# Kernel optimization log

Measured on AMD Instinct MI355X. Metric: run time of the kernel, lower is better.

## Reference

```python
import jax, jax.numpy as jnp
import numpy as np

MAX_DEGREE = 5
NUM_LAYERS = 2


def setup_inputs() -> dict:
    key = jax.random.key(0)
    ks = jax.random.split(key, 10)
    N, F, H, C, E = 200000, 128, 64, 40, 3200000
    x = jax.random.normal(ks[0], (N, F), dtype=jnp.float32)
    edge_index = jax.random.randint(ks[1], (2, E), 0, N, dtype=jnp.int32)
    # torch Linear init ~ U(-1/sqrt(fan_in), 1/sqrt(fan_in)); scaled normals are fine for a baseline
    W1 = jax.random.normal(ks[2], (F, H), dtype=jnp.float32) / np.sqrt(F)
    b1 = jax.random.normal(ks[3], (H,), dtype=jnp.float32) * 0.01
    relW = jax.random.normal(ks[4], (NUM_LAYERS, MAX_DEGREE + 1, H, H), dtype=jnp.float32) / np.sqrt(H)
    relb = jax.random.normal(ks[5], (NUM_LAYERS, MAX_DEGREE + 1, H), dtype=jnp.float32) * 0.01
    Wout = jax.random.normal(ks[6], (H, C), dtype=jnp.float32) / np.sqrt(H)
    bout = jax.random.normal(ks[7], (C,), dtype=jnp.float32) * 0.01
    fuse = jnp.full((NUM_LAYERS,), 1.0 / (NUM_LAYERS + 1), dtype=jnp.float32)
    return {"x": x, "edge_index": edge_index, "W1": W1, "b1": b1,
            "relW": relW, "relb": relb, "Wout": Wout, "bout": bout, "fuse": fuse}


def reference(x, edge_index, W1, b1, relW, relb, Wout, bout, fuse):
    N = x.shape[0]
    src, dst = edge_index[0], edge_index[1]
    loop_mask = (src != dst)  # remove_self_loops
    # degree on target nodes (flow='source_to_target'), clamped to max_degree
    deg = jax.ops.segment_sum(loop_mask.astype(jnp.int32), dst, num_segments=N)
    deg = jnp.clip(deg, 0, MAX_DEGREE)
    node_idx = jnp.arange(N)

    h = jax.nn.relu(x @ W1 + b1)  # dropout is identity in eval mode
    x_first = h
    for i in range(NUM_LAYERS):
        # scatter-add aggregation; self loops added back (root_weight=False)
        msg = jnp.where(loop_mask[:, None], h[src], 0.0)  # [E, H]
        agg = jax.ops.segment_sum(msg, dst, num_segments=N) + h  # [N, H]
        # degree-bucketed linear: compute all 6 buckets, select per node
        all_out = jnp.einsum('nd,kdo->kno', agg, relW[i]) + relb[i][:, None, :]  # [6, N, H]
        conv = all_out[deg, node_idx]  # [N, H]
        h = conv + fuse[i] * x_first
    logits = h @ Wout + bout
    return jax.nn.log_softmax(logits, axis=-1)
```

## Files before the change

kernel.cpp:

```cpp
#include <hip/hip_runtime.h>
#include <cmath>
#include <cstddef>

#define F_IN 128
#define H_DIM 64
#define C_OUT 40
#define MAXDEG 5
#define EPB 16

typedef __attribute__((ext_vector_type(8))) _Float16 half8;
typedef __attribute__((ext_vector_type(4))) _Float16 half4;
typedef __attribute__((ext_vector_type(4))) float fv4;

__device__ __forceinline__ half4 u2h(uint2 u) { return __builtin_bit_cast(half4, u); }
__device__ __forceinline__ uint2 h2u(half4 v) { return __builtin_bit_cast(uint2, v); }


__global__ __launch_bounds__(256) void k_scatter(const int* __restrict__ src,
                                                 const int* __restrict__ dst,
                                                 int E, int NB, int stride,
                                                 int* __restrict__ gcnt,
                                                 unsigned int* __restrict__ ebuf) {
    __shared__ int hist[256];
    __shared__ int base[256];
    int tid = threadIdx.x;
    if (tid < NB) hist[tid] = 0;
    __syncthreads();
    int e0 = blockIdx.x * (256 * EPB);
    int es[EPB], ed[EPB];
#pragma unroll
    for (int i = 0; i < EPB; ++i) {
        int e = e0 + i * 256 + tid;
        int s = -1, d = -1;
        if (e < E) { s = src[e]; d = dst[e]; }
        es[i] = s; ed[i] = d;
        if (d >= 0 && s != d) atomicAdd(&hist[d >> 10], 1);
    }
    __syncthreads();
    if (tid < NB) {
        int c = hist[tid];
        base[tid] = c ? atomicAdd(&gcnt[tid], c) : 0;
        hist[tid] = 0;
    }
    __syncthreads();
#pragma unroll
    for (int i = 0; i < EPB; ++i) {
        int s = es[i], d = ed[i];
        if (d >= 0 && s != d) {
            int b = d >> 10;
            int p = base[b] + atomicAdd(&hist[b], 1);
            if (p < stride)
                ebuf[(size_t)b * stride + p] = ((unsigned)(d & 1023) << 20) | (unsigned)s;
        }
    }
}

__global__ __launch_bounds__(1024) void k_build(const unsigned int* __restrict__ ebuf,
                                                const int* __restrict__ gcnt, int stride, int N,
                                                int* __restrict__ row, int* __restrict__ cnt,
                                                int* __restrict__ col, int* __restrict__ list,
                                                int* __restrict__ listctr) {
    __shared__ int lcnt[1024];
    __shared__ int lcur[1024];
    int bk = blockIdx.x;
    int n0 = bk << 10;
    int tid = threadIdx.x;
    int ebase = bk * stride;
    int ec = min(gcnt[bk], stride);
    int eend = ebase + ec;
    lcnt[tid] = 0;
    __syncthreads();
    for (int e = ebase + tid; e < eend; e += 1024)
        atomicAdd(&lcnt[ebuf[e] >> 20], 1);
    __syncthreads();
    int v = lcnt[tid];
    lcur[tid] = v;
    __syncthreads();
    for (int off = 1; off < 1024; off <<= 1) {
        int t = (tid >= off) ? lcur[tid - off] : 0;
        __syncthreads();
        lcur[tid] += t;
        __syncthreads();
    }
    int ex = lcur[tid] - v;
    __syncthreads();
    lcur[tid] = ebase + ex;
    int n = n0 + tid;
    if (n < N) {
        row[n] = ebase + ex;
        cnt[n] = v;
        if (v < MAXDEG) {
            int p = atomicAdd(listctr, 1);
            list[p] = n;
        }
    }
    __syncthreads();
    for (int e = ebase + tid; e < eend; e += 1024) {
        unsigned edv = ebuf[e];
        int dl = edv >> 20;
        int p = atomicAdd(&lcur[dl], 1);
        col[p] = (int)(edv & 0xFFFFF);
    }
}

__global__ __launch_bounds__(256) void k_lin1(const float* __restrict__ x,
                                              const float* __restrict__ W1,
                                              const float* __restrict__ b1,
                                              _Float16* __restrict__ h, int N) {
    __shared__ _Float16 Wl[4 * 4 * 64 * 8];
    int tid = threadIdx.x;
    for (int idx = tid; idx < 4 * 4 * 64 * 8; idx += 256) {
        int j = idx & 7, ln = (idx >> 3) & 63, ks = (idx >> 9) & 3, t = idx >> 11;
        int k = ks * 32 + (ln >> 4) * 8 + j;
        int n = t * 16 + (ln & 15);
        Wl[idx] = (_Float16)W1[k * H_DIM + n];
    }
    __syncthreads();

    int wave = tid >> 6, lane = tid & 63;
    int tile = blockIdx.x * 4 + wave;
    int row0 = tile * 16;
    if (row0 >= N) return;
    int m = lane & 15, quad = lane >> 4;
    int row = row0 + m;
    if (row >= N) row = N - 1;

    half8 a[4];
    const float* xr = x + (size_t)row * F_IN + quad * 8;
#pragma unroll
    for (int ks = 0; ks < 4; ++ks) {
        fv4 lo = *(const fv4*)(xr + ks * 32);
        fv4 hi = *(const fv4*)(xr + ks * 32 + 4);
        half8 av;
#pragma unroll
        for (int j = 0; j < 4; ++j) av[j] = (_Float16)lo[j];
#pragma unroll
        for (int j = 0; j < 4; ++j) av[4 + j] = (_Float16)hi[j];
        a[ks] = av;
    }

    fv4 acc[4];
#pragma unroll
    for (int t = 0; t < 4; ++t) acc[t] = (fv4){0.f, 0.f, 0.f, 0.f};
#pragma unroll
    for (int ks = 0; ks < 4; ++ks) {
#pragma unroll
        for (int t = 0; t < 4; ++t) {
            half8 b = *(const half8*)&Wl[(((t * 4 + ks) * 64) + lane) * 8];
            acc[t] = __builtin_amdgcn_mfma_f32_16x16x32_f16(a[ks], b, acc[t], 0, 0, 0);
        }
    }
#pragma unroll
    for (int t = 0; t < 4; ++t) {
        int n = t * 16 + m;
        float bias = b1[n];
#pragma unroll
        for (int reg = 0; reg < 4; ++reg) {
            int r = row0 + quad * 4 + reg;
            if (r < N) {
                float v = acc[t][reg] + bias;
                h[(size_t)r * H_DIM + n] = (_Float16)fmaxf(v, 0.f);
            }
        }
    }
}

__global__ void k_agg(const _Float16* __restrict__ hin, const int* __restrict__ row,
                      const int* __restrict__ cnt, const int* __restrict__ col,
                      _Float16* __restrict__ agg, int N) {
    int gid = blockIdx.x * blockDim.x + threadIdx.x;
    int n = gid >> 6, lane = gid & 63;
    if (n >= N) return;
    int g = lane >> 4;
    int f = lane & 15;
    int base = row[n];
    int c = cnt[n];
    const uint2* hv = (const uint2*)hin;
    half4 acc = u2h((uint2){0u, 0u});
    for (int j0 = 0; j0 < c; j0 += 64) {
        int idx = j0 + lane;
        int myc = (idx < c) ? col[base + idx] : 0;
        int mm = min(64, c - j0);
        int t = 0;
        for (; t + 8 <= mm; t += 8) {
            int s0 = __shfl(myc, t + g);
            int s1 = __shfl(myc, t + 4 + g);
            uint2 u0 = hv[(size_t)s0 * 16 + f];
            uint2 u1 = hv[(size_t)s1 * 16 + f];
            acc += u2h(u0);
            acc += u2h(u1);
        }
        for (; t < mm; t += 4) {
            int e = t + g;
            bool val = (e < mm);
            int s = __shfl(myc, val ? e : 0);
            uint2 u = hv[(size_t)(val ? s : n) * 16 + f];
            if (!val) u = (uint2){0u, 0u};
            acc += u2h(u);
        }
    }
    {
        uint2 t1 = h2u(acc);
        t1.x = __shfl_xor(t1.x, 16); t1.y = __shfl_xor(t1.y, 16);
        acc += u2h(t1);
        uint2 t2 = h2u(acc);
        t2.x = __shfl_xor(t2.x, 32); t2.y = __shfl_xor(t2.y, 32);
        acc += u2h(t2);
    }
    acc += u2h(hv[(size_t)n * 16 + f]);
    if (g == 0)
        ((uint2*)agg)[(size_t)n * 16 + f] = h2u(acc);
}

__global__ __launch_bounds__(256) void k_bucket(const _Float16* __restrict__ agg,
                                                const float* __restrict__ relW,
                                                const float* __restrict__ relb,
                                                const float* __restrict__ fuse, int layer,
                                                const _Float16* __restrict__ xfirst,
                                                _Float16* __restrict__ h, int N) {
    __shared__ _Float16 Wl[4 * 2 * 64 * 8];
    const float* W = relW + (size_t)(layer * 6 + MAXDEG) * (H_DIM * H_DIM);
    int tid = threadIdx.x;
    for (int idx = tid; idx < 4 * 2 * 64 * 8; idx += 256) {
        int j = idx & 7, ln = (idx >> 3) & 63, ks = (idx >> 9) & 1, t = idx >> 10;
        int k = ks * 32 + (ln >> 4) * 8 + j;
        int n = t * 16 + (ln & 15);
        Wl[idx] = (_Float16)W[k * H_DIM + n];
    }
    __syncthreads();

    int wave = tid >> 6, lane = tid & 63;
    int tile = blockIdx.x * 4 + wave;
    int row0 = tile * 16;
    if (row0 >= N) return;
    int m = lane & 15, quad = lane >> 4;
    int row = row0 + m;
    if (row >= N) row = N - 1;

    half8 a[2];
#pragma unroll
    for (int ks = 0; ks < 2; ++ks)
        a[ks] = *(const half8*)(agg + (size_t)row * H_DIM + ks * 32 + quad * 8);

    fv4 acc[4];
#pragma unroll
    for (int t = 0; t < 4; ++t) acc[t] = (fv4){0.f, 0.f, 0.f, 0.f};
#pragma unroll
    for (int ks = 0; ks < 2; ++ks) {
#pragma unroll
        for (int t = 0; t < 4; ++t) {
            half8 b = *(const half8*)&Wl[(((t * 2 + ks) * 64) + lane) * 8];
            acc[t] = __builtin_amdgcn_mfma_f32_16x16x32_f16(a[ks], b, acc[t], 0, 0, 0);
        }
    }
    float fu = fuse[layer];
    const float* bias = relb + (layer * 6 + MAXDEG) * H_DIM;
#pragma unroll
    for (int t = 0; t < 4; ++t) {
        int n = t * 16 + m;
        float bv = bias[n];
#pragma unroll
        for (int reg = 0; reg < 4; ++reg) {
            int r = row0 + quad * 4 + reg;
            if (r < N) {
                float v = acc[t][reg] + bv + fu * (float)xfirst[(size_t)r * H_DIM + n];
                h[(size_t)r * H_DIM + n] = (_Float16)v;
            }
        }
    }
}

__global__ void k_fixup(const _Float16* __restrict__ agg, const int* __restrict__ list,
                        const int* __restrict__ listctr, const int* __restrict__ cnt,
                        const float* __restrict__ relW, const float* __restrict__ relb,
                        const float* __restrict__ fuse, int layer,
                        const _Float16* __restrict__ xfirst,
                        _Float16* __restrict__ h) {
    int gid = blockIdx.x * blockDim.x + threadIdx.x;
    int wave = gid >> 6, lane = gid & 63;
    int nwaves = (gridDim.x * blockDim.x) >> 6;
    int M = *listctr;
    float fu = fuse[layer];
    for (int i = wave; i < M; i += nwaves) {
        int n = list[i];
        int d = cnt[n];
        const float* W = relW + (size_t)(layer * 6 + d) * (H_DIM * H_DIM);
        float a = (float)agg[(size_t)n * H_DIM + lane];
        float acc = relb[(layer * 6 + d) * H_DIM + lane];
#pragma unroll 16
        for (int k = 0; k < 64; ++k)
            acc = fmaf(__shfl(a, k), W[k * H_DIM + lane], acc);
        acc += fu * (float)xfirst[(size_t)n * H_DIM + lane];
        h[(size_t)n * H_DIM + lane] = (_Float16)acc;
    }
}

__global__ __launch_bounds__(256) void k_out(const _Float16* __restrict__ h,
                                             const float* __restrict__ Wout,
                                             const float* __restrict__ bout,
                                             float* __restrict__ out, int N) {
    __shared__ _Float16 Wl[3 * 2 * 64 * 8];
    int tid = threadIdx.x;
    for (int idx = tid; idx < 3 * 2 * 64 * 8; idx += 256) {
        int j = idx & 7, ln = (idx >> 3) & 63, ks = (idx >> 9) & 1, t = idx >> 10;
        int k = ks * 32 + (ln >> 4) * 8 + j;
        int n = t * 16 + (ln & 15);
        Wl[idx] = (n < C_OUT) ? (_Float16)Wout[k * C_OUT + n] : (_Float16)0.f;
    }
    __syncthreads();

    int wave = tid >> 6, lane = tid & 63;
    int tile = blockIdx.x * 4 + wave;
    int row0 = tile * 16;
    if (row0 >= N) return;
    int m = lane & 15, quad = lane >> 4;
    int row = row0 + m;
    if (row >= N) row = N - 1;

    half8 a[2];
#pragma unroll
    for (int ks = 0; ks < 2; ++ks)
        a[ks] = *(const half8*)(h + (size_t)row * H_DIM + ks * 32 + quad * 8);

    fv4 acc[3];
#pragma unroll
    for (int t = 0; t < 3; ++t) acc[t] = (fv4){0.f, 0.f, 0.f, 0.f};
#pragma unroll
    for (int ks = 0; ks < 2; ++ks) {
#pragma unroll
        for (int t = 0; t < 3; ++t) {
            half8 b = *(const half8*)&Wl[(((t * 2 + ks) * 64) + lane) * 8];
            acc[t] = __builtin_amdgcn_mfma_f32_16x16x32_f16(a[ks], b, acc[t], 0, 0, 0);
        }
    }
    bool v2 = (m < 8);
    float b0 = bout[m], b1v = bout[16 + m], b2v = v2 ? bout[32 + m] : 0.f;
#pragma unroll
    for (int reg = 0; reg < 4; ++reg) {
        int r = row0 + quad * 4 + reg;
        float l0 = acc[0][reg] + b0;
        float l1 = acc[1][reg] + b1v;
        float l2 = v2 ? (acc[2][reg] + b2v) : -INFINITY;
        float mx = fmaxf(fmaxf(l0, l1), l2);
#pragma unroll
        for (int off = 1; off < 16; off <<= 1) mx = fmaxf(mx, __shfl_xor(mx, off));
        float s = expf(l0 - mx) + expf(l1 - mx) + (v2 ? expf(l2 - mx) : 0.f);
#pragma unroll
        for (int off = 1; off < 16; off <<= 1) s += __shfl_xor(s, off);
        float ls = logf(s);
        if (r < N) {
            out[(size_t)r * C_OUT + m] = l0 - mx - ls;
            out[(size_t)r * C_OUT + 16 + m] = l1 - mx - ls;
            if (v2) out[(size_t)r * C_OUT + 32 + m] = l2 - mx - ls;
        }
    }
}

extern "C" void kernel_launch(void* const* d_in, const int* in_sizes, int n_in,
                              void* d_out, int out_size, void* d_ws, size_t ws_size,
                              hipStream_t stream) {
    const float* x    = (const float*)d_in[0];
    const int*   ei   = (const int*)d_in[1];
    const float* W1   = (const float*)d_in[2];
    const float* b1   = (const float*)d_in[3];
    const float* relW = (const float*)d_in[4];
    const float* relb = (const float*)d_in[5];
    const float* Wout = (const float*)d_in[6];
    const float* bout = (const float*)d_in[7];
    const float* fuse = (const float*)d_in[8];
    float* out = (float*)d_out;

    int N = in_sizes[0] / F_IN;
    int E = in_sizes[1] / 2;
    const int* src = ei;
    const int* dst = ei + E;
    int NB = (N + 1023) >> 10;
    int mean = (E + NB - 1) / NB;
    int stride = mean + mean / 8 + 512;

    char* w = (char*)d_ws;
    auto alloc = [&](size_t bytes) {
        char* p = w;
        w += (bytes + 255) & ~(size_t)255;
        return p;
    };
    int* cnt     = (int*)alloc((size_t)N * 4);
    int* row     = (int*)alloc((size_t)N * 4);
    int* list    = (int*)alloc((size_t)N * 4);
    int* listctr = (int*)alloc(256);
    int* gcnt    = (int*)alloc(1024 * 4);
    int* col     = (int*)alloc((size_t)NB * stride * 4);
    _Float16* h0   = (_Float16*)alloc((size_t)N * H_DIM * 2);
    _Float16* h1   = (_Float16*)alloc((size_t)N * H_DIM * 2);
    _Float16* aggb = (_Float16*)alloc((size_t)N * H_DIM * 2);
    unsigned int* ebuf = (unsigned int*)h0;

    hipMemsetAsync(gcnt, 0, 1024 * 4, stream);
    hipMemsetAsync(listctr, 0, 4, stream);

    k_scatter<<<(E + 256 * EPB - 1) / (256 * EPB), 256, 0, stream>>>(src, dst, E, NB, stride, gcnt, ebuf);
    k_build<<<NB, 1024, 0, stream>>>(ebuf, gcnt, stride, N, row, cnt, col, list, listctr);

    int tiles = (N + 15) / 16;
    int gblk = (tiles + 3) / 4;
    int ablk = ((size_t)N * 64 + 255) / 256;

    k_lin1<<<gblk, 256, 0, stream>>>(x, W1, b1, h0, N);

    k_agg<<<ablk, 256, 0, stream>>>(h0, row, cnt, col, aggb, N);
    k_bucket<<<gblk, 256, 0, stream>>>(aggb, relW, relb, fuse, 0, h0, h1, N);
    k_fixup<<<16, 256, 0, stream>>>(aggb, list, listctr, cnt, relW, relb, fuse, 0, h0, h1);

    k_agg<<<ablk, 256, 0, stream>>>(h1, row, cnt, col, aggb, N);
    k_bucket<<<gblk, 256, 0, stream>>>(aggb, relW, relb, fuse, 1, h0, h1, N);
    k_fixup<<<16, 256, 0, stream>>>(aggb, list, listctr, cnt, relW, relb, fuse, 1, h0, h1);

    k_out<<<gblk, 256, 0, stream>>>(h1, Wout, bout, out, N);
}
```

Measured before the change: 532.4 us.

## Fuse low-degree fixup into bucket GEMM, fuse output head, and repack aggregation

The separate fixup kernels are removed. Each bucket block now patches its own low-degree rows using a shared-memory list, so the global list and its atomics are gone. The final layer's bucket transform is fused with the output projection and log-softmax through a shared-memory staging tile, which drops the h1 round trip and one launch. Aggregation now gives each wave four nodes (16 lanes each) and pads with a zero sentinel row to avoid shuffle reductions. CSR bins shrink to 512 nodes. The cost is per-block serial fixup work and lane divergence when nodes in a wave have uneven degrees.

```diff
diff --git a/kernel.cpp b/kernel.cpp
--- a/kernel.cpp
+++ b/kernel.cpp
@@ -21,10 +21,10 @@
                                                  int E, int NB, int stride,
                                                  int* __restrict__ gcnt,
                                                  unsigned int* __restrict__ ebuf) {
-    __shared__ int hist[256];
-    __shared__ int base[256];
+    __shared__ int hist[512];
+    __shared__ int base[512];
     int tid = threadIdx.x;
-    if (tid < NB) hist[tid] = 0;
+    for (int i = tid; i < NB; i += 256) hist[i] = 0;
     __syncthreads();
     int e0 = blockIdx.x * (256 * EPB);
     int es[EPB], ed[EPB];
@@ -34,49 +34,48 @@
         int s = -1, d = -1;
         if (e < E) { s = src[e]; d = dst[e]; }
         es[i] = s; ed[i] = d;
-        if (d >= 0 && s != d) atomicAdd(&hist[d >> 10], 1);
-    }
-    __syncthreads();
-    if (tid < NB) {
-        int c = hist[tid];
-        base[tid] = c ? atomicAdd(&gcnt[tid], c) : 0;
-        hist[tid] = 0;
+        if (d >= 0 && s != d) atomicAdd(&hist[d >> 9], 1);
+    }
+    __syncthreads();
+    for (int i = tid; i < NB; i += 256) {
+        int c = hist[i];
+        base[i] = c ? atomicAdd(&gcnt[i], c) : 0;
+        hist[i] = 0;
     }
     __syncthreads();
 #pragma unroll
     for (int i = 0; i < EPB; ++i) {
         int s = es[i], d = ed[i];
         if (d >= 0 && s != d) {
-            int b = d >> 10;
+            int b = d >> 9;
             int p = base[b] + atomicAdd(&hist[b], 1);
             if (p < stride)
-                ebuf[(size_t)b * stride + p] = ((unsigned)(d & 1023) << 20) | (unsigned)s;
-        }
-    }
-}
-
-__global__ __launch_bounds__(1024) void k_build(const unsigned int* __restrict__ ebuf,
-                                                const int* __restrict__ gcnt, int stride, int N,
-                                                int* __restrict__ row, int* __restrict__ cnt,
-                                                int* __restrict__ col, int* __restrict__ list,
-                                                int* __restrict__ listctr) {
-    __shared__ int lcnt[1024];
-    __shared__ int lcur[1024];
+                ebuf[(size_t)b * stride + p] = ((unsigned)(d & 511) << 20) | (unsigned)s;
+        }
+    }
+}
+
+__global__ __launch_bounds__(512) void k_build(const unsigned int* __restrict__ ebuf,
+                                               const int* __restrict__ gcnt, int stride, int N,
+                                               int* __restrict__ row, int* __restrict__ cnt,
+                                               int* __restrict__ col) {
+    __shared__ int lcnt[512];
+    __shared__ int lcur[512];
     int bk = blockIdx.x;
-    int n0 = bk << 10;
+    int n0 = bk << 9;
     int tid = threadIdx.x;
     int ebase = bk * stride;
     int ec = min(gcnt[bk], stride);
     int eend = ebase + ec;
     lcnt[tid] = 0;
     __syncthreads();
-    for (int e = ebase + tid; e < eend; e += 1024)
+    for (int e = ebase + tid; e < eend; e += 512)
         atomicAdd(&lcnt[ebuf[e] >> 20], 1);
     __syncthreads();
     int v = lcnt[tid];
     lcur[tid] = v;
     __syncthreads();
-    for (int off = 1; off < 1024; off <<= 1) {
+    for (int off = 1; off < 512; off <<= 1) {
         int t = (tid >= off) ? lcur[tid - off] : 0;
         __syncthreads();
         lcur[tid] += t;
@@ -89,13 +88,9 @@
     if (n < N) {
         row[n] = ebase + ex;
         cnt[n] = v;
-        if (v < MAXDEG) {
-            int p = atomicAdd(listctr, 1);
-            list[p] = n;
-        }
-    }
-    __syncthreads();
-    for (int e = ebase + tid; e < eend; e += 1024) {
+    }
+    __syncthreads();
+    for (int e = ebase + tid; e < eend; e += 512) {
         unsigned edv = ebuf[e];
         int dl = edv >> 20;
         int p = atomicAdd(&lcur[dl], 1);
@@ -106,9 +101,14 @@
 __global__ __launch_bounds__(256) void k_lin1(const float* __restrict__ x,
                                               const float* __restrict__ W1,
                                               const float* __restrict__ b1,
-                                              _Float16* __restrict__ h, int N) {
+                                              _Float16* __restrict__ h,
+                                              _Float16* __restrict__ hz2, int N) {
     __shared__ _Float16 Wl[4 * 4 * 64 * 8];
     int tid = threadIdx.x;
+    if (blockIdx.x == 0 && tid < 64) {
+        h[(size_t)N * H_DIM + tid] = (_Float16)0.f;
+        hz2[(size_t)N * H_DIM + tid] = (_Float16)0.f;
+    }
     for (int idx = tid; idx < 4 * 4 * 64 * 8; idx += 256) {
         int j = idx & 7, ln = (idx >> 3) & 63, ks = (idx >> 9) & 3, t = idx >> 11;
         int k = ks * 32 + (ln >> 4) * 8 + j;
@@ -168,59 +168,60 @@
 __global__ void k_agg(const _Float16* __restrict__ hin, const int* __restrict__ row,
                       const int* __restrict__ cnt, const int* __restrict__ col,
                       _Float16* __restrict__ agg, int N) {
-    int gid = blockIdx.x * blockDim.x + threadIdx.x;
-    int n = gid >> 6, lane = gid & 63;
-    if (n >= N) return;
-    int g = lane >> 4;
-    int f = lane & 15;
-    int base = row[n];
-    int c = cnt[n];
+    int wid = (blockIdx.x * blockDim.x + threadIdx.x) >> 6;
+    int lane = threadIdx.x & 63;
+    int g = lane >> 4, fl = lane & 15, gl = g << 4;
+    int n = wid * 4 + g;
+    bool nv = (n < N);
+    int nn = nv ? n : (N - 1);
+    int base = row[nn];
+    int c = nv ? cnt[nn] : 0;
     const uint2* hv = (const uint2*)hin;
+    int cmax = c;
+    cmax = max(cmax, __shfl_xor(cmax, 16));
+    cmax = max(cmax, __shfl_xor(cmax, 32));
     half4 acc = u2h((uint2){0u, 0u});
-    for (int j0 = 0; j0 < c; j0 += 64) {
-        int idx = j0 + lane;
-        int myc = (idx < c) ? col[base + idx] : 0;
-        int mm = min(64, c - j0);
+    for (int j0 = 0; j0 < cmax; j0 += 16) {
+        int idx = j0 + fl;
+        int myc = (idx < c) ? col[base + idx] : N;
+        int tmax = min(16, cmax - j0);
         int t = 0;
-        for (; t + 8 <= mm; t += 8) {
-            int s0 = __shfl(myc, t + g);
-            int s1 = __shfl(myc, t + 4 + g);
-            uint2 u0 = hv[(size_t)s0 * 16 + f];
-            uint2 u1 = hv[(size_t)s1 * 16 + f];
-            acc += u2h(u0);
-            acc += u2h(u1);
-        }
-        for (; t < mm; t += 4) {
-            int e = t + g;
-            bool val = (e < mm);
-            int s = __shfl(myc, val ? e : 0);
-            uint2 u = hv[(size_t)(val ? s : n) * 16 + f];
-            if (!val) u = (uint2){0u, 0u};
-            acc += u2h(u);
-        }
-    }
-    {
-        uint2 t1 = h2u(acc);
-        t1.x = __shfl_xor(t1.x, 16); t1.y = __shfl_xor(t1.y, 16);
-        acc += u2h(t1);
-        uint2 t2 = h2u(acc);
-        t2.x = __shfl_xor(t2.x, 32); t2.y = __shfl_xor(t2.y, 32);
-        acc += u2h(t2);
-    }
-    acc += u2h(hv[(size_t)n * 16 + f]);
-    if (g == 0)
-        ((uint2*)agg)[(size_t)n * 16 + f] = h2u(acc);
+        for (; t + 4 <= tmax; t += 4) {
+            int s0 = __shfl(myc, gl + t);
+            int s1 = __shfl(myc, gl + t + 1);
+            int s2 = __shfl(myc, gl + t + 2);
+            int s3 = __shfl(myc, gl + t + 3);
+            uint2 u0 = hv[(size_t)s0 * 16 + fl];
+            uint2 u1 = hv[(size_t)s1 * 16 + fl];
+            uint2 u2 = hv[(size_t)s2 * 16 + fl];
+            uint2 u3 = hv[(size_t)s3 * 16 + fl];
+            half4 p01 = u2h(u0) + u2h(u1);
+            half4 p23 = u2h(u2) + u2h(u3);
+            acc += (p01 + p23);
+        }
+        for (; t < tmax; ++t) {
+            int s = __shfl(myc, gl + t);
+            acc += u2h(hv[(size_t)s * 16 + fl]);
+        }
+    }
+    acc += u2h(hv[(size_t)nn * 16 + fl]);
+    if (nv)
+        ((uint2*)agg)[(size_t)nn * 16 + fl] = h2u(acc);
 }
 
 __global__ __launch_bounds__(256) void k_bucket(const _Float16* __restrict__ agg,
+                                                const int* __restrict__ cnt,
                                                 const float* __restrict__ relW,
                                                 const float* __restrict__ relb,
                                                 const float* __restrict__ fuse, int layer,
                                                 const _Float16* __restrict__ xfirst,
                                                 _Float16* __restrict__ h, int N) {
     __shared__ _Float16 Wl[4 * 2 * 64 * 8];
+    __shared__ int flist[64];
+    __shared__ int fn;
     const float* W = relW + (size_t)(layer * 6 + MAXDEG) * (H_DIM * H_DIM);
     int tid = threadIdx.x;
+    if (tid == 0) fn = 0;
     for (int idx = tid; idx < 4 * 2 * 64 * 8; idx += 256) {
         int j = idx & 7, ln = (idx >> 3) & 63, ks = (idx >> 9) & 1, t = idx >> 10;
         int k = ks * 32 + (ln >> 4) * 8 + j;
@@ -230,12 +231,12 @@
     __syncthreads();
 
     int wave = tid >> 6, lane = tid & 63;
-    int tile = blockIdx.x * 4 + wave;
-    int row0 = tile * 16;
-    if (row0 >= N) return;
+    int row0 = blockIdx.x * 64 + wave * 16;
     int m = lane & 15, quad = lane >> 4;
     int row = row0 + m;
     if (row >= N) row = N - 1;
+    float fu = fuse[layer];
+    const float* bias = relb + (layer * 6 + MAXDEG) * H_DIM;
 
     half8 a[2];
 #pragma unroll
@@ -246,15 +247,29 @@
 #pragma unroll
     for (int t = 0; t < 4; ++t) acc[t] = (fv4){0.f, 0.f, 0.f, 0.f};
 #pragma unroll
-    for (int ks = 0; ks < 2; ++ks) {
+    for (int ks = 0; ks < 2; ++ks)
 #pragma unroll
         for (int t = 0; t < 4; ++t) {
             half8 b = *(const half8*)&Wl[(((t * 2 + ks) * 64) + lane) * 8];
             acc[t] = __builtin_amdgcn_mfma_f32_16x16x32_f16(a[ks], b, acc[t], 0, 0, 0);
         }
-    }
-    float fu = fuse[layer];
-    const float* bias = relb + (layer * 6 + MAXDEG) * H_DIM;
+
+    int cr[4];
+#pragma unroll
+    for (int reg = 0; reg < 4; ++reg) {
+        int r = row0 + quad * 4 + reg;
+        cr[reg] = (r < N) ? cnt[r] : MAXDEG;
+    }
+    if (m == 0) {
+#pragma unroll
+        for (int reg = 0; reg < 4; ++reg) {
+            int r = row0 + quad * 4 + reg;
+            if (r < N && cr[reg] < MAXDEG) {
+                int p = atomicAdd(&fn, 1);
+                if (p < 64) flist[p] = wave * 16 + quad * 4 + reg;
+            }
+        }
+    }
 #pragma unroll
     for (int t = 0; t < 4; ++t) {
         int n = t * 16 + m;
@@ -262,85 +277,153 @@
 #pragma unroll
         for (int reg = 0; reg < 4; ++reg) {
             int r = row0 + quad * 4 + reg;
-            if (r < N) {
+            if (r < N && cr[reg] >= MAXDEG) {
                 float v = acc[t][reg] + bv + fu * (float)xfirst[(size_t)r * H_DIM + n];
                 h[(size_t)r * H_DIM + n] = (_Float16)v;
             }
         }
     }
-}
-
-__global__ void k_fixup(const _Float16* __restrict__ agg, const int* __restrict__ list,
-                        const int* __restrict__ listctr, const int* __restrict__ cnt,
-                        const float* __restrict__ relW, const float* __restrict__ relb,
-                        const float* __restrict__ fuse, int layer,
-                        const _Float16* __restrict__ xfirst,
-                        _Float16* __restrict__ h) {
-    int gid = blockIdx.x * blockDim.x + threadIdx.x;
-    int wave = gid >> 6, lane = gid & 63;
-    int nwaves = (gridDim.x * blockDim.x) >> 6;
-    int M = *listctr;
-    float fu = fuse[layer];
-    for (int i = wave; i < M; i += nwaves) {
-        int n = list[i];
-        int d = cnt[n];
-        const float* W = relW + (size_t)(layer * 6 + d) * (H_DIM * H_DIM);
-        float a = (float)agg[(size_t)n * H_DIM + lane];
-        float acc = relb[(layer * 6 + d) * H_DIM + lane];
-#pragma unroll 16
+    __syncthreads();
+    int M = min(fn, 64);
+    for (int i = wave; i < M; i += 4) {
+        int rl = flist[i];
+        int r = blockIdx.x * 64 + rl;
+        int d = cnt[r];
+        const float* Wd = relW + (size_t)(layer * 6 + d) * (H_DIM * H_DIM);
+        float av = (float)agg[(size_t)r * H_DIM + lane];
+        float accf = relb[(layer * 6 + d) * H_DIM + lane];
         for (int k = 0; k < 64; ++k)
-            acc = fmaf(__shfl(a, k), W[k * H_DIM + lane], acc);
-        acc += fu * (float)xfirst[(size_t)n * H_DIM + lane];
-        h[(size_t)n * H_DIM + lane] = (_Float16)acc;
-    }
-}
-
-__global__ __launch_bounds__(256) void k_out(const _Float16* __restrict__ h,
-                                             const float* __restrict__ Wout,
-                                             const float* __restrict__ bout,
-                                             float* __restrict__ out, int N) {
-    __shared__ _Float16 Wl[3 * 2 * 64 * 8];
+            accf = fmaf(__shfl(av, k), Wd[k * H_DIM + lane], accf);
+        accf += fu * (float)xfirst[(size_t)r * H_DIM + lane];
+        h[(size_t)r * H_DIM + lane] = (_Float16)accf;
+    }
+}
+
+#define HB 80
+__global__ __launch_bounds__(256) void k_bucket_out(const _Float16* __restrict__ agg,
+                                                    const int* __restrict__ cnt,
+                                                    const float* __restrict__ relW,
+                                                    const float* __restrict__ relb,
+                                                    const float* __restrict__ fuse,
+                                                    const _Float16* __restrict__ xfirst,
+                                                    const float* __restrict__ Wout,
+                                                    const float* __restrict__ bout,
+                                                    float* __restrict__ out, int N) {
+    __shared__ _Float16 Wl[4 * 2 * 64 * 8];
+    __shared__ _Float16 Wo[3 * 2 * 64 * 8];
+    __shared__ _Float16 hbuf[64 * HB];
+    __shared__ int flist[64];
+    __shared__ int fn;
+    const int layer = 1;
+    const float* W = relW + (size_t)(layer * 6 + MAXDEG) * (H_DIM * H_DIM);
     int tid = threadIdx.x;
+    if (tid == 0) fn = 0;
+    for (int idx = tid; idx < 4 * 2 * 64 * 8; idx += 256) {
+        int j = idx & 7, ln = (idx >> 3) & 63, ks = (idx >> 9) & 1, t = idx >> 10;
+        int k = ks * 32 + (ln >> 4) * 8 + j;
+        int n = t * 16 + (ln & 15);
+        Wl[idx] = (_Float16)W[k * H_DIM + n];
+    }
     for (int idx = tid; idx < 3 * 2 * 64 * 8; idx += 256) {
         int j = idx & 7, ln = (idx >> 3) & 63, ks = (idx >> 9) & 1, t = idx >> 10;
         int k = ks * 32 + (ln >> 4) * 8 + j;
         int n = t * 16 + (ln & 15);
-        Wl[idx] = (n < C_OUT) ? (_Float16)Wout[k * C_OUT + n] : (_Float16)0.f;
+        Wo[idx] = (n < C_OUT) ? (_Float16)Wout[k * C_OUT + n] : (_Float16)0.f;
     }
     __syncthreads();
 
     int wave = tid >> 6, lane = tid & 63;
-    int tile = blockIdx.x * 4 + wave;
-    int row0 = tile * 16;
-    if (row0 >= N) return;
+    int row0 = blockIdx.x * 64 + wave * 16;
     int m = lane & 15, quad = lane >> 4;
     int row = row0 + m;
     if (row >= N) row = N - 1;
+    float fu = fuse[layer];
+    const float* bias = relb + (layer * 6 + MAXDEG) * H_DIM;
 
     half8 a[2];
 #pragma unroll
     for (int ks = 0; ks < 2; ++ks)
-        a[ks] = *(const half8*)(h + (size_t)row * H_DIM + ks * 32 + quad * 8);
-
-    fv4 acc[3];
-#pragma unroll
-    for (int t = 0; t < 3; ++t) acc[t] = (fv4){0.f, 0.f, 0.f, 0.f};
-#pragma unroll
-    for (int ks = 0; ks < 2; ++ks) {
-#pragma unroll
-        for (int t = 0; t < 3; ++t) {
+        a[ks] = *(const half8*)(agg + (size_t)row * H_DIM + ks * 32 + quad * 8);
+
+    fv4 acc[4];
+#pragma unroll
+    for (int t = 0; t < 4; ++t) acc[t] = (fv4){0.f, 0.f, 0.f, 0.f};
+#pragma unroll
+    for (int ks = 0; ks < 2; ++ks)
+#pragma unroll
+        for (int t = 0; t < 4; ++t) {
             half8 b = *(const half8*)&Wl[(((t * 2 + ks) * 64) + lane) * 8];
             acc[t] = __builtin_amdgcn_mfma_f32_16x16x32_f16(a[ks], b, acc[t], 0, 0, 0);
         }
-    }
+
+    int cr[4];
+#pragma unroll
+    for (int reg = 0; reg < 4; ++reg) {
+        int r = row0 + quad * 4 + reg;
+        cr[reg] = (r < N) ? cnt[r] : MAXDEG;
+    }
+    if (m == 0) {
+#pragma unroll
+        for (int reg = 0; reg < 4; ++reg) {
+            int r = row0 + quad * 4 + reg;
+            if (r < N && cr[reg] < MAXDEG) {
+                int p = atomicAdd(&fn, 1);
+                if (p < 64) flist[p] = wave * 16 + quad * 4 + reg;
+            }
+        }
+    }
+#pragma unroll
+    for (int t = 0; t < 4; ++t) {
+        int n = t * 16 + m;
+        float bv = bias[n];
+#pragma unroll
+        for (int reg = 0; reg < 4; ++reg) {
+            int r = row0 + quad * 4 + reg;
+            int rc = (r < N) ? r : (N - 1);
+            float v = acc[t][reg] + bv + fu * (float)xfirst[(size_t)rc * H_DIM + n];
+            int rl = wave * 16 + quad * 4 + reg;
+            hbuf[rl * HB + n] = (_Float16)v;
+        }
+    }
+    __syncthreads();
+    int M = min(fn, 64);
+    for (int i = wave; i < M; i += 4) {
+        int rl = flist[i];
+        int r = blockIdx.x * 64 + rl;
+        int d = cnt[r];
+        const float* Wd = relW + (size_t)(layer * 6 + d) * (H_DIM * H_DIM);
+        float av = (float)agg[(size_t)r * H_DIM + lane];
+        float accf = relb[(layer * 6 + d) * H_DIM + lane];
+        for (int k = 0; k < 64; ++k)
+            accf = fmaf(__shfl(av, k), Wd[k * H_DIM + lane], accf);
+        accf += fu * (float)xfirst[(size_t)r * H_DIM + lane];
+        hbuf[rl * HB + lane] = (_Float16)accf;
+    }
+    __syncthreads();
+
+    half8 ao[2];
+#pragma unroll
+    for (int ks = 0; ks < 2; ++ks)
+        ao[ks] = *(const half8*)&hbuf[(wave * 16 + m) * HB + ks * 32 + quad * 8];
+
+    fv4 lacc[3];
+#pragma unroll
+    for (int t = 0; t < 3; ++t) lacc[t] = (fv4){0.f, 0.f, 0.f, 0.f};
+#pragma unroll
+    for (int ks = 0; ks < 2; ++ks)
+#pragma unroll
+        for (int t = 0; t < 3; ++t) {
+            half8 b = *(const half8*)&Wo[(((t * 2 + ks) * 64) + lane) * 8];
+            lacc[t] = __builtin_amdgcn_mfma_f32_16x16x32_f16(ao[ks], b, lacc[t], 0, 0, 0);
+        }
     bool v2 = (m < 8);
     float b0 = bout[m], b1v = bout[16 + m], b2v = v2 ? bout[32 + m] : 0.f;
 #pragma unroll
     for (int reg = 0; reg < 4; ++reg) {
         int r = row0 + quad * 4 + reg;
-        float l0 = acc[0][reg] + b0;
-        float l1 = acc[1][reg] + b1v;
-        float l2 = v2 ? (acc[2][reg] + b2v) : -INFINITY;
+        float l0 = lacc[0][reg] + b0;
+        float l1 = lacc[1][reg] + b1v;
+        float l2 = v2 ? (lacc[2][reg] + b2v) : -INFINITY;
         float mx = fmaxf(fmaxf(l0, l1), l2);
 #pragma unroll
         for (int off = 1; off < 16; off <<= 1) mx = fmaxf(mx, __shfl_xor(mx, off));
@@ -374,7 +457,7 @@
     int E = in_sizes[1] / 2;
     const int* src = ei;
     const int* dst = ei + E;
-    int NB = (N + 1023) >> 10;
+    int NB = (N + 511) >> 9;
     int mean = (E + NB - 1) / NB;
     int stride = mean + mean / 8 + 512;
 
@@ -384,36 +467,30 @@
         w += (bytes + 255) & ~(size_t)255;
         return p;
     };
-    int* cnt     = (int*)alloc((size_t)N * 4);
-    int* row     = (int*)alloc((size_t)N * 4);
-    int* list    = (int*)alloc((size_t)N * 4);
-    int* listctr = (int*)alloc(256);
-    int* gcnt    = (int*)alloc(1024 * 4);
-    int* col     = (int*)alloc((size_t)NB * stride * 4);
-    _Float16* h0   = (_Float16*)alloc((size_t)N * H_DIM * 2);
-    _Float16* h1   = (_Float16*)alloc((size_t)N * H_DIM * 2);
+    int* cnt  = (int*)alloc((size_t)N * 4);
+    int* row  = (int*)alloc((size_t)N * 4);
+    int* gcnt = (int*)alloc(1024 * 4);
+    int* col  = (int*)alloc((size_t)NB * stride * 4);
+    _Float16* h0   = (_Float16*)alloc((size_t)(N + 1) * H_DIM * 2);
+    _Float16* h1   = (_Float16*)alloc((size_t)(N + 1) * H_DIM * 2);
     _Float16* aggb = (_Float16*)alloc((size_t)N * H_DIM * 2);
     unsigned int* ebuf = (unsigned int*)h0;
 
     hipMemsetAsync(gcnt, 0, 1024 * 4, stream);
-    hipMemsetAsync(listctr, 0, 4, stream);
 
     k_scatter<<<(E + 256 * EPB - 1) / (256 * EPB), 256, 0, stream>>>(src, dst, E, NB, stride, gcnt, ebuf);
-    k_build<<<NB, 1024, 0, stream>>>(ebuf, gcnt, stride, N, row, cnt, col, list, listctr);
+    k_build<<<NB, 512, 0, stream>>>(ebuf, gcnt, stride, N, row, cnt, col);
 
     int tiles = (N + 15) / 16;
     int gblk = (tiles + 3) / 4;
-    int ablk = ((size_t)N * 64 + 255) / 256;
-
-    k_lin1<<<gblk, 256, 0, stream>>>(x, W1, b1, h0, N);
+    int awaves = (N + 3) / 4;
+    int ablk = (awaves * 64 + 255) / 256;
+
+    k_lin1<<<gblk, 256, 0, stream>>>(x, W1, b1, h0, h1, N);
 
     k_agg<<<ablk, 256, 0, stream>>>(h0, row, cnt, col, aggb, N);
-    k_bucket<<<gblk, 256, 0, stream>>>(aggb, relW, relb, fuse, 0, h0, h1, N);
-    k_fixup<<<16, 256, 0, stream>>>(aggb, list, listctr, cnt, relW, relb, fuse, 0, h0, h1);
+    k_bucket<<<gblk, 256, 0, stream>>>(aggb, cnt, relW, relb, fuse, 0, h0, h1, N);
 
     k_agg<<<ablk, 256, 0, stream>>>(h1, row, cnt, col, aggb, N);
-    k_bucket<<<gblk, 256, 0, stream>>>(aggb, relW, relb, fuse, 1, h0, h1, N);
-    k_fixup<<<16, 256, 0, stream>>>(aggb, list, listctr, cnt, relW, relb, fuse, 1, h0, h1);
-
-    k_out<<<gblk, 256, 0, stream>>>(h1, Wout, bout, out, N);
-}
+    k_bucket_out<<<gblk, 256, 0, stream>>>(aggb, cnt, relW, relb, fuse, h0, Wout, bout, out, N);
+}
```

Result: faster. 461.0 us (-13.4%).
